# Optimization experiments

Measured on AMD Instinct MI355X. Metric: run time of the kernel, lower is better.

Reference implementation:

```python
import jax, jax.numpy as jnp
import numpy as np

B = 8192      # batch
F = 20        # sparse features
V = 1000      # vocab per sparse feature
E = 32        # embedding dim
ND = 10       # dense features
IN0 = (F + ND) * E  # 960 total embed dim
T = 2         # tasks
K = 4         # task experts per task
S = 4         # shared experts
D = 512       # expert dim
H = 256       # tower hidden
TEMP = 2.0    # gate temperature
EPS = 1e-5    # batchnorm eps


def setup_inputs() -> dict:
    key = jax.random.key(0)
    ks = iter(jax.random.split(key, 64))
    n = lambda shape, s=0.02: jax.random.normal(next(ks), shape, dtype=jnp.float32) * s
    inp = {
        'sparse_features': jax.random.randint(next(ks), (B, F), 0, V, dtype=jnp.int32),
        'dense_features': jax.random.normal(next(ks), (B, ND), dtype=jnp.float32),
        'emb_tables': n((F, V, E), 0.05),
        'dense_W': n((ND, ND * E)),
        'dense_b': jnp.zeros((ND * E,), jnp.float32),
    }
    for i, ind in enumerate([IN0, D, D]):
        inp[f'l{i}_Wt'] = n((T, K, ind, D))
        inp[f'l{i}_bt'] = jnp.zeros((T, K, D), jnp.float32)
        inp[f'l{i}_Ws'] = n((S, ind, D))
        inp[f'l{i}_bs'] = jnp.zeros((S, D), jnp.float32)
        inp[f'l{i}_Wg'] = n((T, ind, K + S))
        inp[f'l{i}_bg'] = jnp.zeros((T, K + S), jnp.float32)
    inp['tw1'] = n((T, D, H)); inp['tb1'] = jnp.zeros((T, H), jnp.float32)
    inp['bn_g'] = jnp.ones((T, H), jnp.float32); inp['bn_b'] = jnp.zeros((T, H), jnp.float32)
    inp['bn_m'] = jnp.zeros((T, H), jnp.float32); inp['bn_v'] = jnp.ones((T, H), jnp.float32)
    inp['tw2'] = n((T, H, H // 2)); inp['tb2'] = jnp.zeros((T, H // 2), jnp.float32)
    inp['tw3'] = n((T, H // 2)); inp['tb3'] = jnp.zeros((T,), jnp.float32)
    return inp


def _ple_layer(x, Wt, bt, Ws, bs, Wg, bg):
    # x: [B, in]; Wt: [T,K,in,D]; Ws: [S,in,D]; Wg: [T,in,K+S]
    shared = jax.nn.relu(jnp.einsum('bi,sio->bso', x, Ws) + bs)        # [B,S,D]
    task = jax.nn.relu(jnp.einsum('bi,tkio->btko', x, Wt) + bt)        # [B,T,K,D]
    Bn = x.shape[0]
    stack = jnp.concatenate(
        [task, jnp.broadcast_to(shared[:, None], (Bn, T) + shared.shape[1:])], axis=2)  # [B,T,K+S,D]
    gw = jax.nn.softmax((jnp.einsum('bi,tie->bte', x, Wg) + bg) / TEMP, axis=-1)        # [B,T,K+S]
    return jnp.einsum('bte,bted->btd', gw, stack)                      # [B,T,D]


def reference(sparse_features, dense_features, emb_tables, dense_W, dense_b,
              l0_Wt, l0_bt, l0_Ws, l0_bs, l0_Wg, l0_bg,
              l1_Wt, l1_bt, l1_Ws, l1_bs, l1_Wg, l1_bg,
              l2_Wt, l2_bt, l2_Ws, l2_bs, l2_Wg, l2_bg,
              tw1, tb1, bn_g, bn_b, bn_m, bn_v, tw2, tb2, tw3, tb3):
    # embedding: per-feature table lookup then concat with projected dense
    sp = emb_tables[jnp.arange(F)[None, :], sparse_features]           # [B,F,E]
    embed = jnp.concatenate(
        [sp.reshape(sp.shape[0], F * E), dense_features @ dense_W + dense_b], axis=1)  # [B,IN0]

    x = embed
    tout = None
    for (Wt, bt, Ws, bs, Wg, bg) in [
        (l0_Wt, l0_bt, l0_Ws, l0_bs, l0_Wg, l0_bg),
        (l1_Wt, l1_bt, l1_Ws, l1_bs, l1_Wg, l1_bg),
        (l2_Wt, l2_bt, l2_Ws, l2_bs, l2_Wg, l2_bg),
    ]:
        tout = _ple_layer(x, Wt, bt, Ws, bs, Wg, bg)   # [B,T,D]
        x = tout.mean(axis=1)                           # next layer input

    # task towers (eval mode: BN uses running stats, dropout off)
    h = jnp.einsum('btd,tdh->bth', tout, tw1) + tb1
    h = (h - bn_m) / jnp.sqrt(bn_v + EPS) * bn_g + bn_b
    h = jax.nn.relu(h)
    h = jax.nn.relu(jnp.einsum('bth,thg->btg', h, tw2) + tb2)
    logits = jnp.einsum('btg,tg->bt', h, tw3) + tb3     # [B,T]

    ctr = jax.nn.sigmoid(logits[:, 0])
    cvr_raw = jax.nn.sigmoid(logits[:, 1])
    ctcvr = ctr * cvr_raw
    # use_esmm=True -> cvr_pred == ctcvr
    return jnp.stack([ctr, ctcvr, ctcvr])               # [3,B]: ctr, cvr, ctcvr
```

## Files before the change

kernel.cpp:

```cpp
#include <hip/hip_runtime.h>
#include <math.h>

#define Bn 8192
#define INP0 960
#define Dn 512
#define Hn 256
#define TEMP_INV 0.5f

typedef __attribute__((ext_vector_type(8))) short short8;
typedef __attribute__((ext_vector_type(8))) unsigned short ushort8;
typedef __attribute__((ext_vector_type(4))) float f32x4;
typedef __attribute__((ext_vector_type(2))) long lx2;

__device__ __forceinline__ int swz(int x) { return x ^ ((x >> 3) & 0x70); }

__device__ __forceinline__ unsigned short f2bf(float f) {
  unsigned u = __builtin_bit_cast(unsigned, f);
  u += 0x7FFF + ((u >> 16) & 1);
  return (unsigned short)(u >> 16);
}
__device__ __forceinline__ float bf2f(unsigned short s) {
  unsigned u = ((unsigned)s) << 16;
  return __builtin_bit_cast(float, u);
}
__device__ __forceinline__ int pk4fp8(float a, float b, float c, float d) {
  int r = __builtin_amdgcn_cvt_pk_fp8_f32(a, b, 0, 0);
  r = __builtin_amdgcn_cvt_pk_fp8_f32(c, d, r, 1);
  return r;
}
__device__ __forceinline__ void gload16(const void* g, void* l) {
  __builtin_amdgcn_global_load_lds(
      (const __attribute__((address_space(1))) unsigned int*)g,
      (__attribute__((address_space(3))) unsigned int*)l, 16, 0, 0);
}

template <int IN>
__global__ __launch_bounds__(256) void conv_w(const float* __restrict__ Wt,
                                              const float* __restrict__ Ws,
                                              unsigned char* __restrict__ Wbt) {
  __shared__ float T[64][65];
  const int NK = IN / 64;
  int kk = blockIdx.x, dblk = blockIdx.y, e = blockIdx.z;
  int t = threadIdx.x;
  const float* base = (e < 8) ? (Wt + (size_t)e * IN * Dn) : (Ws + (size_t)(e - 8) * IN * Dn);
  int k = t >> 2, dg = t & 3;
  const float* gp = base + (size_t)(kk * 64 + k) * Dn + dblk * 64 + dg * 16;
#pragma unroll
  for (int i = 0; i < 4; ++i) {
    float4 v = *(const float4*)(gp + i * 4);
    T[dg * 16 + i * 4 + 0][k] = v.x;
    T[dg * 16 + i * 4 + 1][k] = v.y;
    T[dg * 16 + i * 4 + 2][k] = v.z;
    T[dg * 16 + i * 4 + 3][k] = v.w;
  }
  __syncthreads();
  int col = t >> 2, gq = t & 3;
  int g = gq ^ ((col >> 1) & 3);
  const float* Tc = T[col];
  int4 o;
  o.x = pk4fp8(Tc[g * 8 + 0] * 16.f, Tc[g * 8 + 1] * 16.f, Tc[g * 8 + 2] * 16.f, Tc[g * 8 + 3] * 16.f);
  o.y = pk4fp8(Tc[g * 8 + 4] * 16.f, Tc[g * 8 + 5] * 16.f, Tc[g * 8 + 6] * 16.f, Tc[g * 8 + 7] * 16.f);
  o.z = pk4fp8(Tc[32 + g * 8 + 0] * 16.f, Tc[32 + g * 8 + 1] * 16.f, Tc[32 + g * 8 + 2] * 16.f, Tc[32 + g * 8 + 3] * 16.f);
  o.w = pk4fp8(Tc[32 + g * 8 + 4] * 16.f, Tc[32 + g * 8 + 5] * 16.f, Tc[32 + g * 8 + 6] * 16.f, Tc[32 + g * 8 + 7] * 16.f);
  *(int4*)(Wbt + (((size_t)(dblk * NK + kk) * 12 + e) << 12) + t * 16) = o;
}

template <int K, int H>
__global__ __launch_bounds__(256) void conv_tw(const float* __restrict__ W,
                                               unsigned short* __restrict__ out) {
  __shared__ float T[64][33];
  int kk = blockIdx.x, hb = blockIdx.y, t = blockIdx.z;
  int tid = threadIdx.x;
  const float* base = W + (size_t)t * K * H;
  int k = tid >> 3, dq = tid & 7;
  const float* gp = base + (size_t)(kk * 32 + k) * H + hb * 64 + dq * 8;
  float4 v0 = *(const float4*)gp, v1 = *(const float4*)(gp + 4);
  T[dq * 8 + 0][k] = v0.x; T[dq * 8 + 1][k] = v0.y; T[dq * 8 + 2][k] = v0.z; T[dq * 8 + 3][k] = v0.w;
  T[dq * 8 + 4][k] = v1.x; T[dq * 8 + 5][k] = v1.y; T[dq * 8 + 6][k] = v1.z; T[dq * 8 + 7][k] = v1.w;
  __syncthreads();
  int L = tid * 16;
  int nat = swz(L);
  int c = nat >> 6, k0 = (nat & 63) >> 1;
  ushort8 o;
#pragma unroll
  for (int u = 0; u < 8; ++u) o[u] = f2bf(T[c][k0 + u]);
  const int NHB = H / 64;
  *(ushort8*)(out + (((size_t)(kk * NHB + hb) * 2 + t) << 11) + (L >> 1)) = o;
}

__global__ __launch_bounds__(256) void embed_kernel(
    const int* __restrict__ sparse, const float* __restrict__ dense,
    const float* __restrict__ emb, const float* __restrict__ dW,
    const float* __restrict__ db,
    unsigned short* __restrict__ xn, unsigned char* __restrict__ xt) {
  int b = blockIdx.x, t = threadIdx.x;
  __shared__ float dfs[10];
  if (t < 10) dfs[t] = dense[b * 10 + t];
  __syncthreads();
  if (t >= 240) return;
  int c = t * 4;
  float v[4];
  if (c < 640) {
    int f = c >> 5, e0 = c & 31;
    int idx = sparse[b * 20 + f];
    const float* ep = emb + ((size_t)f * 1000 + idx) * 32 + e0;
    float4 q = *(const float4*)ep;
    v[0] = q.x; v[1] = q.y; v[2] = q.z; v[3] = q.w;
  } else {
    int j = c - 640;
#pragma unroll
    for (int u = 0; u < 4; ++u) {
      float a = db[j + u];
#pragma unroll
      for (int d = 0; d < 10; ++d) a += dfs[d] * dW[d * 320 + j + u];
      v[u] = a;
    }
  }
  ushort4 pk;
  pk.x = f2bf(v[0]); pk.y = f2bf(v[1]); pk.z = f2bf(v[2]); pk.w = f2bf(v[3]);
  *(ushort4*)(xn + (size_t)b * 960 + c) = pk;
  int col = b & 63;
  int lc = c & 63;
  int ks = lc >> 5, g = (lc & 31) >> 3, j0 = lc & 7;
  int gq = g ^ ((col >> 1) & 3);
  int pos = (col << 6) + (gq << 4) + (ks << 3) + j0;
  int p8 = pk4fp8(v[0] * 16.f, v[1] * 16.f, v[2] * 16.f, v[3] * 16.f);
  *(int*)(xt + (((size_t)(c >> 6) * 128 + (b >> 6)) << 12) + pos) = p8;
}

template <int IN>
__global__ __launch_bounds__(256) void gate_kernel(
    const unsigned short* __restrict__ x, const float* __restrict__ Wg,
    const float* __restrict__ bg, float* __restrict__ gates) {
  int tid = threadIdx.x;
  int wv = tid >> 6, lane = tid & 63;
  int b = blockIdx.x * 4 + wv;
  int e = lane & 15, t = e >> 3, eg = e & 7;
  int slice = lane >> 4;
  const unsigned short* xr = x + (size_t)b * IN;
  const float* wr = Wg + (size_t)t * IN * 8 + eg;
  float p = 0.f;
  for (int i = slice * (IN / 4); i < (slice + 1) * (IN / 4); i += 4) {
    ushort4 xv = *(const ushort4*)(xr + i);
    p += bf2f(xv.x) * wr[(size_t)(i + 0) * 8];
    p += bf2f(xv.y) * wr[(size_t)(i + 1) * 8];
    p += bf2f(xv.z) * wr[(size_t)(i + 2) * 8];
    p += bf2f(xv.w) * wr[(size_t)(i + 3) * 8];
  }
  p += __shfl_xor(p, 32);
  p += __shfl_xor(p, 16);
  float z = (p + bg[t * 8 + eg]) * TEMP_INV;
  float m = z;
  m = fmaxf(m, __shfl_xor(m, 1)); m = fmaxf(m, __shfl_xor(m, 2)); m = fmaxf(m, __shfl_xor(m, 4));
  float ex = expf(z - m);
  float s = ex;
  s += __shfl_xor(s, 1); s += __shfl_xor(s, 2); s += __shfl_xor(s, 4);
  if (lane < 16) gates[(size_t)b * 16 + lane] = ex / s;
}

#define GSH 0
#define OUTS 4096
#define SB 22528
#define STG 53248

template <int IN, int MODE>
__global__ __launch_bounds__(768, 3) void ple_mfma(
    const unsigned char* __restrict__ xt, const float* __restrict__ gates,
    const unsigned char* __restrict__ Wbt,
    const float* __restrict__ btb, const float* __restrict__ bsh,
    unsigned short* __restrict__ outn, unsigned char* __restrict__ outt8,
    unsigned short* __restrict__ outtb) {
  __shared__ __align__(16) char smem[129024];
  const int NK = IN / 64;
  int tid = threadIdx.x;
  int wv = tid >> 6, lane = tid & 63;
  int r = lane & 15, g = lane >> 4;
  int s = blockIdx.x;
  int dblk = s & 7, bblk = s >> 3;
  int b0 = bblk * 64, d0 = dblk * 64;

  if (tid < 256)
    *(float4*)(smem + GSH + tid * 16) = *(const float4*)(gates + (size_t)b0 * 16 + tid * 4);

  f32x4 acc[4][4];
#pragma unroll
  for (int i = 0; i < 4; ++i)
#pragma unroll
    for (int j = 0; j < 4; ++j) acc[i][j] = f32x4{0.f, 0.f, 0.f, 0.f};

  const unsigned char* xchunk = xt + ((size_t)bblk << 12);
  const unsigned char* wchunk = Wbt + (size_t)(dblk * NK) * 49152;

  auto stage = [&](int t, char* lb) {
    const unsigned char* ws = wchunk + (size_t)t * 49152;
#pragma unroll
    for (int i = 0; i < 4; ++i)
      gload16(ws + tid * 16 + i * 12288, lb + tid * 16 + i * 12288);
    if (tid < 256)
      gload16(xchunk + (size_t)t * (128 * 4096) + tid * 16, lb + 49152 + tid * 16);
  };

  stage(0, smem + SB);

  for (int kk = 0; kk < NK; ++kk) {
    asm volatile("s_waitcnt vmcnt(0)" ::: "memory");
    __builtin_amdgcn_s_barrier();
    if (kk + 1 < NK) stage(kk + 1, smem + SB + ((kk + 1) & 1) * STG);
    {
      const char* lb = smem + SB + (kk & 1) * STG;
      const char* xb = lb + 49152;
      const char* wb = lb + (wv << 12);
      int base = (r << 6) + ((g ^ ((r >> 1) & 3)) << 4);
      lx2 A[4], B[4];
#pragma unroll
      for (int rt = 0; rt < 4; ++rt) A[rt] = *(const lx2*)(xb + rt * 1024 + base);
#pragma unroll
      for (int ct = 0; ct < 4; ++ct) B[ct] = *(const lx2*)(wb + ct * 1024 + base);
#pragma unroll
      for (int rt = 0; rt < 4; ++rt)
#pragma unroll
        for (int ct = 0; ct < 4; ++ct)
          acc[rt][ct] = __builtin_amdgcn_mfma_f32_16x16x32_fp8_fp8(A[rt][0], B[ct][0], acc[rt][ct], 0, 0, 0);
#pragma unroll
      for (int rt = 0; rt < 4; ++rt)
#pragma unroll
        for (int ct = 0; ct < 4; ++ct)
          acc[rt][ct] = __builtin_amdgcn_mfma_f32_16x16x32_fp8_fp8(A[rt][1], B[ct][1], acc[rt][ct], 0, 0, 0);
    }
  }
  __syncthreads();

  {
    const float* bp = (wv < 8) ? (btb + wv * Dn) : (bsh + (wv - 8) * Dn);
    float bias[4];
#pragma unroll
    for (int ct = 0; ct < 4; ++ct) bias[ct] = bp[d0 + ct * 16 + r];
    char* ex = smem + SB + (wv << 12);
#pragma unroll
    for (int rt = 0; rt < 4; ++rt)
#pragma unroll
      for (int ct = 0; ct < 4; ++ct) {
        float v0 = fmaxf(acc[rt][ct][0] * 0.00390625f + bias[ct], 0.f) * 16.f;
        float v1 = fmaxf(acc[rt][ct][1] * 0.00390625f + bias[ct], 0.f) * 16.f;
        float v2 = fmaxf(acc[rt][ct][2] * 0.00390625f + bias[ct], 0.f) * 16.f;
        float v3 = fmaxf(acc[rt][ct][3] * 0.00390625f + bias[ct], 0.f) * 16.f;
        int col = ct * 16 + r;
        int off = (col << 6) + rt * 16 + g * 4;
        off ^= (col & 7) << 3;
        *(int*)(ex + off) = pk4fp8(v0, v1, v2, v3);
      }
  }
  __syncthreads();

  if (tid < 512) {
    int col = tid & 63, q = tid >> 6;
    int exoff = ((col << 6) + (q << 3)) ^ ((col & 7) << 3);
    long v[12];
#pragma unroll
    for (int e = 0; e < 12; ++e)
      v[e] = *(const long*)(smem + SB + (e << 12) + exoff);
    unsigned short* os0 = (unsigned short*)(smem + OUTS);
    unsigned short* os1 = os0 + 64 * 72;
#pragma unroll
    for (int half = 0; half < 2; ++half) {
#pragma unroll
      for (int jj = 0; jj < 4; ++jj) {
        int row = (q << 3) + half * 4 + jj;
        const float* gp = (const float*)(smem + GSH + (row << 6));
        float4 ga = ((const float4*)gp)[0];
        float4 gb = ((const float4*)gp)[1];
        float4 gc = ((const float4*)gp)[2];
        float4 gd = ((const float4*)gp)[3];
        float f[12];
#pragma unroll
        for (int e = 0; e < 12; ++e) {
          unsigned w32 = (unsigned)(v[e] >> (half * 32));
          f[e] = __builtin_amdgcn_cvt_f32_fp8((int)(w32 >> (jj * 8)), 0);
        }
        float s0 = ga.x * f[0] + ga.y * f[1] + ga.z * f[2] + ga.w * f[3] +
                   gb.x * f[8] + gb.y * f[9] + gb.z * f[10] + gb.w * f[11];
        float s1 = gc.x * f[4] + gc.y * f[5] + gc.z * f[6] + gc.w * f[7] +
                   gd.x * f[8] + gd.y * f[9] + gd.z * f[10] + gd.w * f[11];
        os0[row * 72 + col] = f2bf(s0 * 0.0625f);
        os1[row * 72 + col] = f2bf(s1 * 0.0625f);
      }
    }
  }
  __syncthreads();

  if (tid < 512) {
    int row = tid >> 3, cq = tid & 7;
    const unsigned short* os0 = (const unsigned short*)(smem + OUTS) + row * 72 + cq * 8;
    const unsigned short* os1 = os0 + 64 * 72;
    ushort8 p0 = *(const ushort8*)os0, p1 = *(const ushort8*)os1;
    int b = b0 + row, d = d0 + cq * 8;
    if (MODE == 0) {
      float m[8];
      ushort8 pk;
#pragma unroll
      for (int u = 0; u < 8; ++u) {
        m[u] = 0.5f * (bf2f((unsigned short)p0[u]) + bf2f((unsigned short)p1[u]));
        pk[u] = f2bf(m[u]);
      }
      *(ushort8*)(outn + (size_t)b * Dn + d) = pk;
      int lk = d & 63;
      int ks = lk >> 5, g2 = (lk & 31) >> 3;
      int gq = g2 ^ ((row >> 1) & 3);
      int pos = (row << 6) + (gq << 4) + (ks << 3);
      int2 o8;
      o8.x = pk4fp8(m[0] * 16.f, m[1] * 16.f, m[2] * 16.f, m[3] * 16.f);
      o8.y = pk4fp8(m[4] * 16.f, m[5] * 16.f, m[6] * 16.f, m[7] * 16.f);
      *(int2*)(outt8 + (((size_t)dblk * 128 + bblk) << 12) + pos) = o8;
    } else {
      int kk2 = d >> 5;
      int nat = (row << 6) + ((d & 31) << 1);
      *(ushort8*)(outtb + (((size_t)(0 * 16 + kk2) * 128 + bblk) << 11) + (swz(nat) >> 1)) = p0;
      *(ushort8*)(outtb + (((size_t)(1 * 16 + kk2) * 128 + bblk) << 11) + (swz(nat) >> 1)) = p1;
    }
  }
}

#define TWBUF 36864
#define H1OFF 73728

__global__ __launch_bounds__(512) void tower_mfma(
    const unsigned short* __restrict__ toutT,
    const unsigned short* __restrict__ twbt1, const unsigned short* __restrict__ twbt2,
    const float* __restrict__ tb1,
    const float* __restrict__ bng, const float* __restrict__ bnb,
    const float* __restrict__ bnm, const float* __restrict__ bnv,
    const float* __restrict__ tb2, const float* __restrict__ tw3,
    const float* __restrict__ tb3, float* __restrict__ out) {
  __shared__ __align__(16) char smem[106496];
  int tid = threadIdx.x;
  int wv = tid >> 6, lane = tid & 63, r = lane & 15, g = lane >> 4;
  int blk = blockIdx.x;
  int bblk = blk >> 1, sub = blk & 1;
  int b0 = blk * 32;
  char* h1t = smem + H1OFF;

  int t1 = wv >> 2, hb = wv & 3;
  f32x4 acc[2][4];
#pragma unroll
  for (int i = 0; i < 2; ++i)
#pragma unroll
    for (int j = 0; j < 4; ++j) acc[i][j] = f32x4{0.f, 0.f, 0.f, 0.f};

  auto stage1 = [&](int t, char* lb) {
#pragma unroll
    for (int i = 0; i < 4; ++i)
      gload16((const char*)twbt1 + (size_t)t * 32768 + tid * 16 + i * 8192,
              lb + tid * 16 + i * 8192);
    if (tid < 256) {
      int tt = tid >> 7, off = (tid & 127) * 16;
      gload16((const char*)toutT + (((size_t)(tt * 16 + t) * 128 + bblk) << 12) + sub * 2048 + off,
              lb + 32768 + tt * 2048 + off);
    }
  };

  stage1(0, smem);
  __syncthreads();
  int cur = 0;
  for (int kk = 0; kk < 16; ++kk) {
    if (kk + 1 < 16) stage1(kk + 1, smem + (cur ^ 1) * TWBUF);
    {
      const char* lb = smem + cur * TWBUF;
      const char* wb = lb + (hb * 2 + t1) * 4096;
      const char* xb = lb + 32768 + t1 * 2048;
      short8 a[2], bfr[4];
#pragma unroll
      for (int rt = 0; rt < 2; ++rt)
        a[rt] = *(const short8*)(xb + swz(((rt * 16 + r) << 6) + (g << 4)));
#pragma unroll
      for (int ct = 0; ct < 4; ++ct)
        bfr[ct] = *(const short8*)(wb + swz(((ct * 16 + r) << 6) + (g << 4)));
#pragma unroll
      for (int rt = 0; rt < 2; ++rt)
#pragma unroll
        for (int ct = 0; ct < 4; ++ct)
          acc[rt][ct] = __builtin_amdgcn_mfma_f32_16x16x32_bf16(a[rt], bfr[ct], acc[rt][ct], 0, 0, 0);
    }
    __syncthreads();
    cur ^= 1;
  }

  {
#pragma unroll
    for (int ct = 0; ct < 4; ++ct) {
      int h = hb * 64 + ct * 16 + r;
      int idx = t1 * 256 + h;
      float inv = rsqrtf(bnv[idx] + 1e-5f) * bng[idx];
      float mu = bnm[idx], be = bnb[idx], bias = tb1[idx];
      int kk2 = h >> 5, kloc = h & 31;
      char* tile = h1t + (t1 * 8 + kk2) * 2048;
#pragma unroll
      for (int rt = 0; rt < 2; ++rt)
#pragma unroll
        for (int j = 0; j < 4; ++j) {
          int lr = rt * 16 + g * 4 + j;
          float v = acc[rt][ct][j] + bias;
          v = (v - mu) * inv + be;
          v = fmaxf(v, 0.f);
          *(unsigned short*)(tile + swz((lr << 6) + (kloc << 1))) = f2bf(v);
        }
    }
  }
  __syncthreads();

  float* h2x = (float*)smem;
  if (wv < 4) {
    int t2 = wv >> 1, hb2 = wv & 1;
    f32x4 acc2[2][4];
#pragma unroll
    for (int i = 0; i < 2; ++i)
#pragma unroll
      for (int j = 0; j < 4; ++j) acc2[i][j] = f32x4{0.f, 0.f, 0.f, 0.f};
    for (int kk = 0; kk < 8; ++kk) {
      const char* xb = h1t + (t2 * 8 + kk) * 2048;
      const char* wb = (const char*)twbt2 + ((kk * 2 + hb2) * 2 + t2) * 4096;
      short8 a[2], bfr[4];
#pragma unroll
      for (int rt = 0; rt < 2; ++rt)
        a[rt] = *(const short8*)(xb + swz(((rt * 16 + r) << 6) + (g << 4)));
#pragma unroll
      for (int ct = 0; ct < 4; ++ct)
        bfr[ct] = *(const short8*)(wb + swz(((ct * 16 + r) << 6) + (g << 4)));
#pragma unroll
      for (int rt = 0; rt < 2; ++rt)
#pragma unroll
        for (int ct = 0; ct < 4; ++ct)
          acc2[rt][ct] = __builtin_amdgcn_mfma_f32_16x16x32_bf16(a[rt], bfr[ct], acc2[rt][ct], 0, 0, 0);
    }
#pragma unroll
    for (int ct = 0; ct < 4; ++ct) {
      int col = hb2 * 64 + ct * 16 + r;
      float bias = tb2[t2 * 128 + col];
#pragma unroll
      for (int rt = 0; rt < 2; ++rt)
#pragma unroll
        for (int j = 0; j < 4; ++j) {
          int lr = rt * 16 + g * 4 + j;
          h2x[(t2 * 32 + lr) * 129 + col] = fmaxf(acc2[rt][ct][j] + bias, 0.f);
        }
    }
  }
  __syncthreads();

  float* lgs = (float*)(smem + 40960);
  if (tid < 64) {
    int t3 = tid >> 5, lr = tid & 31;
    const float* hr = h2x + (t3 * 32 + lr) * 129;
    const float* w3 = tw3 + t3 * 128;
    float s = 0.f;
#pragma unroll 8
    for (int i = 0; i < 128; ++i) s += hr[i] * w3[i];
    lgs[t3 * 32 + lr] = s + tb3[t3];
  }
  __syncthreads();
  if (tid < 32) {
    int b = b0 + tid;
    float ctr = 1.f / (1.f + expf(-lgs[tid]));
    float cvr = 1.f / (1.f + expf(-lgs[32 + tid]));
    float cc = ctr * cvr;
    out[b] = ctr;
    out[Bn + b] = cc;
    out[2 * Bn + b] = cc;
  }
}

extern "C" void kernel_launch(void* const* d_in, const int* in_sizes, int n_in,
                              void* d_out, int out_size, void* d_ws, size_t ws_size,
                              hipStream_t stream) {
  const int* sparse   = (const int*)d_in[0];
  const float* dense  = (const float*)d_in[1];
  const float* emb    = (const float*)d_in[2];
  const float* dW     = (const float*)d_in[3];
  const float* db     = (const float*)d_in[4];
  const float* Wt[3]  = {(const float*)d_in[5],  (const float*)d_in[11], (const float*)d_in[17]};
  const float* btb[3] = {(const float*)d_in[6],  (const float*)d_in[12], (const float*)d_in[18]};
  const float* Wsh[3] = {(const float*)d_in[7],  (const float*)d_in[13], (const float*)d_in[19]};
  const float* bsh[3] = {(const float*)d_in[8],  (const float*)d_in[14], (const float*)d_in[20]};
  const float* Wg[3]  = {(const float*)d_in[9],  (const float*)d_in[15], (const float*)d_in[21]};
  const float* bg[3]  = {(const float*)d_in[10], (const float*)d_in[16], (const float*)d_in[22]};
  const float* tw1 = (const float*)d_in[23];
  const float* tb1 = (const float*)d_in[24];
  const float* bng = (const float*)d_in[25];
  const float* bnb = (const float*)d_in[26];
  const float* bnm = (const float*)d_in[27];
  const float* bnv = (const float*)d_in[28];
  const float* tw2 = (const float*)d_in[29];
  const float* tb2 = (const float*)d_in[30];
  const float* tw3 = (const float*)d_in[31];
  const float* tb3 = (const float*)d_in[32];

  unsigned short* x0n = (unsigned short*)d_ws;
  unsigned short* x1n = x0n + (size_t)Bn * 960;
  unsigned short* toutT = x1n + (size_t)Bn * 512;
  float* gatesB = (float*)(toutT + (size_t)Bn * 1024);
  unsigned short* twbt1 = (unsigned short*)(gatesB + (size_t)Bn * 16);
  unsigned short* twbt2 = twbt1 + (size_t)2 * 512 * 256;
  unsigned char* x0t = (unsigned char*)(twbt2 + (size_t)2 * 256 * 128);
  unsigned char* x1t = x0t + (size_t)Bn * 960;
  unsigned char* Wbt = x1t + (size_t)Bn * 512;
  unsigned short* x2n = x0n;
  unsigned char* x2t = x0t;

  conv_tw<512, 256><<<dim3(16, 4, 2), 256, 0, stream>>>(tw1, twbt1);
  conv_tw<256, 128><<<dim3(8, 2, 2), 256, 0, stream>>>(tw2, twbt2);

  conv_w<960><<<dim3(15, 8, 12), 256, 0, stream>>>(Wt[0], Wsh[0], Wbt);
  embed_kernel<<<Bn, 256, 0, stream>>>(sparse, dense, emb, dW, db, x0n, x0t);
  gate_kernel<960><<<Bn / 4, 256, 0, stream>>>(x0n, Wg[0], bg[0], gatesB);
  ple_mfma<960, 0><<<1024, 768, 0, stream>>>(x0t, gatesB, Wbt, btb[0], bsh[0], x1n, x1t, nullptr);

  conv_w<512><<<dim3(8, 8, 12), 256, 0, stream>>>(Wt[1], Wsh[1], Wbt);
  gate_kernel<512><<<Bn / 4, 256, 0, stream>>>(x1n, Wg[1], bg[1], gatesB);
  ple_mfma<512, 0><<<1024, 768, 0, stream>>>(x1t, gatesB, Wbt, btb[1], bsh[1], x2n, x2t, nullptr);

  conv_w<512><<<dim3(8, 8, 12), 256, 0, stream>>>(Wt[2], Wsh[2], Wbt);
  gate_kernel<512><<<Bn / 4, 256, 0, stream>>>(x2n, Wg[2], bg[2], gatesB);
  ple_mfma<512, 1><<<1024, 768, 0, stream>>>(x2t, gatesB, Wbt, btb[2], bsh[2], nullptr, nullptr, toutT);

  tower_mfma<<<256, 512, 0, stream>>>(toutT, twbt1, twbt2, tb1, bng, bnb, bnm, bnv,
                                      tb2, tw3, tb3, (float*)d_out);
}
```

Measured before the change: 296.7 us.

## Pre-transpose gate weights to bf16, batch embed rows, use bf16 expert staging

```diff
diff --git a/kernel.cpp b/kernel.cpp
--- a/kernel.cpp
+++ b/kernel.cpp
@@ -63,6 +63,14 @@
   o.z = pk4fp8(Tc[32 + g * 8 + 0] * 16.f, Tc[32 + g * 8 + 1] * 16.f, Tc[32 + g * 8 + 2] * 16.f, Tc[32 + g * 8 + 3] * 16.f);
   o.w = pk4fp8(Tc[32 + g * 8 + 4] * 16.f, Tc[32 + g * 8 + 5] * 16.f, Tc[32 + g * 8 + 6] * 16.f, Tc[32 + g * 8 + 7] * 16.f);
   *(int4*)(Wbt + (((size_t)(dblk * NK + kk) * 12 + e) << 12) + t * 16) = o;
+}
+
+__global__ __launch_bounds__(64) void conv_wg(const float* __restrict__ Wg,
+                                              unsigned short* __restrict__ out, int IN) {
+  int i = blockIdx.x * 64 + threadIdx.x;
+  int e = blockIdx.y;
+  int t = e >> 3, eg = e & 7;
+  if (i < IN) out[(size_t)e * IN + i] = f2bf(Wg[((size_t)t * IN + i) * 8 + eg]);
 }
 
 template <int K, int H>
@@ -93,62 +101,67 @@
     const float* __restrict__ emb, const float* __restrict__ dW,
     const float* __restrict__ db,
     unsigned short* __restrict__ xn, unsigned char* __restrict__ xt) {
-  int b = blockIdx.x, t = threadIdx.x;
-  __shared__ float dfs[10];
-  if (t < 10) dfs[t] = dense[b * 10 + t];
+  int b0 = blockIdx.x * 4, t = threadIdx.x;
+  __shared__ float dfs[4][10];
+  if (t < 40) dfs[t / 10][t % 10] = dense[(b0 + t / 10) * 10 + t % 10];
   __syncthreads();
   if (t >= 240) return;
   int c = t * 4;
-  float v[4];
-  if (c < 640) {
-    int f = c >> 5, e0 = c & 31;
-    int idx = sparse[b * 20 + f];
-    const float* ep = emb + ((size_t)f * 1000 + idx) * 32 + e0;
-    float4 q = *(const float4*)ep;
-    v[0] = q.x; v[1] = q.y; v[2] = q.z; v[3] = q.w;
-  } else {
-    int j = c - 640;
-#pragma unroll
-    for (int u = 0; u < 4; ++u) {
-      float a = db[j + u];
-#pragma unroll
-      for (int d = 0; d < 10; ++d) a += dfs[d] * dW[d * 320 + j + u];
-      v[u] = a;
-    }
-  }
-  ushort4 pk;
-  pk.x = f2bf(v[0]); pk.y = f2bf(v[1]); pk.z = f2bf(v[2]); pk.w = f2bf(v[3]);
-  *(ushort4*)(xn + (size_t)b * 960 + c) = pk;
-  int col = b & 63;
-  int lc = c & 63;
-  int ks = lc >> 5, g = (lc & 31) >> 3, j0 = lc & 7;
-  int gq = g ^ ((col >> 1) & 3);
-  int pos = (col << 6) + (gq << 4) + (ks << 3) + j0;
-  int p8 = pk4fp8(v[0] * 16.f, v[1] * 16.f, v[2] * 16.f, v[3] * 16.f);
-  *(int*)(xt + (((size_t)(c >> 6) * 128 + (b >> 6)) << 12) + pos) = p8;
+#pragma unroll 1
+  for (int r = 0; r < 4; ++r) {
+    int b = b0 + r;
+    float v[4];
+    if (c < 640) {
+      int f = c >> 5, e0 = c & 31;
+      int idx = sparse[b * 20 + f];
+      const float* ep = emb + ((size_t)f * 1000 + idx) * 32 + e0;
+      float4 q = *(const float4*)ep;
+      v[0] = q.x; v[1] = q.y; v[2] = q.z; v[3] = q.w;
+    } else {
+      int j = c - 640;
+#pragma unroll
+      for (int u = 0; u < 4; ++u) {
+        float a = db[j + u];
+#pragma unroll
+        for (int d = 0; d < 10; ++d) a += dfs[r][d] * dW[d * 320 + j + u];
+        v[u] = a;
+      }
+    }
+    ushort4 pk;
+    pk.x = f2bf(v[0]); pk.y = f2bf(v[1]); pk.z = f2bf(v[2]); pk.w = f2bf(v[3]);
+    *(ushort4*)(xn + (size_t)b * 960 + c) = pk;
+    int col = b & 63;
+    int lc = c & 63;
+    int ks = lc >> 5, g = (lc & 31) >> 3, j0 = lc & 7;
+    int gq = g ^ ((col >> 1) & 3);
+    int pos = (col << 6) + (gq << 4) + (ks << 3) + j0;
+    int p8 = pk4fp8(v[0] * 16.f, v[1] * 16.f, v[2] * 16.f, v[3] * 16.f);
+    *(int*)(xt + (((size_t)(c >> 6) * 128 + (b >> 6)) << 12) + pos) = p8;
+  }
 }
 
 template <int IN>
 __global__ __launch_bounds__(256) void gate_kernel(
-    const unsigned short* __restrict__ x, const float* __restrict__ Wg,
+    const unsigned short* __restrict__ x, const unsigned short* __restrict__ wgb,
     const float* __restrict__ bg, float* __restrict__ gates) {
   int tid = threadIdx.x;
   int wv = tid >> 6, lane = tid & 63;
   int b = blockIdx.x * 4 + wv;
-  int e = lane & 15, t = e >> 3, eg = e & 7;
-  int slice = lane >> 4;
-  const unsigned short* xr = x + (size_t)b * IN;
-  const float* wr = Wg + (size_t)t * IN * 8 + eg;
+  int e = lane & 15, slice = lane >> 4;
+  const unsigned short* xr = x + (size_t)b * IN + slice * (IN / 4);
+  const unsigned short* wr = wgb + (size_t)e * IN + slice * (IN / 4);
   float p = 0.f;
-  for (int i = slice * (IN / 4); i < (slice + 1) * (IN / 4); i += 4) {
-    ushort4 xv = *(const ushort4*)(xr + i);
-    p += bf2f(xv.x) * wr[(size_t)(i + 0) * 8];
-    p += bf2f(xv.y) * wr[(size_t)(i + 1) * 8];
-    p += bf2f(xv.z) * wr[(size_t)(i + 2) * 8];
-    p += bf2f(xv.w) * wr[(size_t)(i + 3) * 8];
-  }
+#pragma unroll 2
+  for (int i = 0; i < IN / 4; i += 8) {
+    short8 xv = *(const short8*)(xr + i);
+    short8 wv2 = *(const short8*)(wr + i);
+#pragma unroll
+    for (int u = 0; u < 8; ++u)
+      p += bf2f((unsigned short)xv[u]) * bf2f((unsigned short)wv2[u]);
+  }
+  p += __shfl_xor(p, 16);
   p += __shfl_xor(p, 32);
-  p += __shfl_xor(p, 16);
+  int t = e >> 3, eg = e & 7;
   float z = (p + bg[t * 8 + eg]) * TEMP_INV;
   float m = z;
   m = fmaxf(m, __shfl_xor(m, 1)); m = fmaxf(m, __shfl_xor(m, 2)); m = fmaxf(m, __shfl_xor(m, 4));
@@ -235,55 +248,50 @@
     float bias[4];
 #pragma unroll
     for (int ct = 0; ct < 4; ++ct) bias[ct] = bp[d0 + ct * 16 + r];
-    char* ex = smem + SB + (wv << 12);
+    char* ex = smem + SB + (wv << 13);
 #pragma unroll
     for (int rt = 0; rt < 4; ++rt)
 #pragma unroll
       for (int ct = 0; ct < 4; ++ct) {
-        float v0 = fmaxf(acc[rt][ct][0] * 0.00390625f + bias[ct], 0.f) * 16.f;
-        float v1 = fmaxf(acc[rt][ct][1] * 0.00390625f + bias[ct], 0.f) * 16.f;
-        float v2 = fmaxf(acc[rt][ct][2] * 0.00390625f + bias[ct], 0.f) * 16.f;
-        float v3 = fmaxf(acc[rt][ct][3] * 0.00390625f + bias[ct], 0.f) * 16.f;
+        float v0 = fmaxf(acc[rt][ct][0] * 0.00390625f + bias[ct], 0.f);
+        float v1 = fmaxf(acc[rt][ct][1] * 0.00390625f + bias[ct], 0.f);
+        float v2 = fmaxf(acc[rt][ct][2] * 0.00390625f + bias[ct], 0.f);
+        float v3 = fmaxf(acc[rt][ct][3] * 0.00390625f + bias[ct], 0.f);
+        uint2 pk;
+        pk.x = (unsigned)f2bf(v0) | ((unsigned)f2bf(v1) << 16);
+        pk.y = (unsigned)f2bf(v2) | ((unsigned)f2bf(v3) << 16);
         int col = ct * 16 + r;
-        int off = (col << 6) + rt * 16 + g * 4;
-        off ^= (col & 7) << 3;
-        *(int*)(ex + off) = pk4fp8(v0, v1, v2, v3);
+        *(uint2*)(ex + swz(col * 128 + rt * 32 + g * 8)) = pk;
       }
   }
   __syncthreads();
 
   if (tid < 512) {
     int col = tid & 63, q = tid >> 6;
-    int exoff = ((col << 6) + (q << 3)) ^ ((col & 7) << 3);
-    long v[12];
+    short8 v[12];
 #pragma unroll
     for (int e = 0; e < 12; ++e)
-      v[e] = *(const long*)(smem + SB + (e << 12) + exoff);
+      v[e] = *(const short8*)(smem + SB + (e << 13) + swz(col * 128 + q * 16));
     unsigned short* os0 = (unsigned short*)(smem + OUTS);
     unsigned short* os1 = os0 + 64 * 72;
 #pragma unroll
-    for (int half = 0; half < 2; ++half) {
-#pragma unroll
-      for (int jj = 0; jj < 4; ++jj) {
-        int row = (q << 3) + half * 4 + jj;
-        const float* gp = (const float*)(smem + GSH + (row << 6));
-        float4 ga = ((const float4*)gp)[0];
-        float4 gb = ((const float4*)gp)[1];
-        float4 gc = ((const float4*)gp)[2];
-        float4 gd = ((const float4*)gp)[3];
-        float f[12];
-#pragma unroll
-        for (int e = 0; e < 12; ++e) {
-          unsigned w32 = (unsigned)(v[e] >> (half * 32));
-          f[e] = __builtin_amdgcn_cvt_f32_fp8((int)(w32 >> (jj * 8)), 0);
-        }
-        float s0 = ga.x * f[0] + ga.y * f[1] + ga.z * f[2] + ga.w * f[3] +
-                   gb.x * f[8] + gb.y * f[9] + gb.z * f[10] + gb.w * f[11];
-        float s1 = gc.x * f[4] + gc.y * f[5] + gc.z * f[6] + gc.w * f[7] +
-                   gd.x * f[8] + gd.y * f[9] + gd.z * f[10] + gd.w * f[11];
-        os0[row * 72 + col] = f2bf(s0 * 0.0625f);
-        os1[row * 72 + col] = f2bf(s1 * 0.0625f);
-      }
+    for (int jj = 0; jj < 8; ++jj) {
+      int row = q * 8 + jj;
+      const float* gp = (const float*)(smem + GSH + (row << 6));
+      float4 ga = ((const float4*)gp)[0];
+      float4 gb = ((const float4*)gp)[1];
+      float4 gc = ((const float4*)gp)[2];
+      float4 gd = ((const float4*)gp)[3];
+      float sh0 = bf2f((unsigned short)v[8][jj]), sh1 = bf2f((unsigned short)v[9][jj]);
+      float sh2 = bf2f((unsigned short)v[10][jj]), sh3 = bf2f((unsigned short)v[11][jj]);
+      float s0 = ga.x * bf2f((unsigned short)v[0][jj]) + ga.y * bf2f((unsigned short)v[1][jj]) +
+                 ga.z * bf2f((unsigned short)v[2][jj]) + ga.w * bf2f((unsigned short)v[3][jj]) +
+                 gb.x * sh0 + gb.y * sh1 + gb.z * sh2 + gb.w * sh3;
+      float s1 = gc.x * bf2f((unsigned short)v[4][jj]) + gc.y * bf2f((unsigned short)v[5][jj]) +
+                 gc.z * bf2f((unsigned short)v[6][jj]) + gc.w * bf2f((unsigned short)v[7][jj]) +
+                 gd.x * sh0 + gd.y * sh1 + gd.z * sh2 + gd.w * sh3;
+      os0[row * 72 + col] = f2bf(s0);
+      os1[row * 72 + col] = f2bf(s1);
     }
   }
   __syncthreads();
@@ -502,23 +510,29 @@
   unsigned char* x0t = (unsigned char*)(twbt2 + (size_t)2 * 256 * 128);
   unsigned char* x1t = x0t + (size_t)Bn * 960;
   unsigned char* Wbt = x1t + (size_t)Bn * 512;
+  unsigned short* wgb0 = (unsigned short*)(Wbt + (size_t)6 * 1024 * 1024);
+  unsigned short* wgb1 = wgb0 + (size_t)16 * 960;
+  unsigned short* wgb2 = wgb1 + (size_t)16 * 512;
   unsigned short* x2n = x0n;
   unsigned char* x2t = x0t;
 
   conv_tw<512, 256><<<dim3(16, 4, 2), 256, 0, stream>>>(tw1, twbt1);
   conv_tw<256, 128><<<dim3(8, 2, 2), 256, 0, stream>>>(tw2, twbt2);
+  conv_wg<<<dim3(15, 16), 64, 0, stream>>>(Wg[0], wgb0, 960);
+  conv_wg<<<dim3(8, 16), 64, 0, stream>>>(Wg[1], wgb1, 512);
+  conv_wg<<<dim3(8, 16), 64, 0, stream>>>(Wg[2], wgb2, 512);
 
   conv_w<960><<<dim3(15, 8, 12), 256, 0, stream>>>(Wt[0], Wsh[0], Wbt);
-  embed_kernel<<<Bn, 256, 0, stream>>>(sparse, dense, emb, dW, db, x0n, x0t);
-  gate_kernel<960><<<Bn / 4, 256, 0, stream>>>(x0n, Wg[0], bg[0], gatesB);
+  embed_kernel<<<Bn / 4, 256, 0, stream>>>(sparse, dense, emb, dW, db, x0n, x0t);
+  gate_kernel<960><<<Bn / 4, 256, 0, stream>>>(x0n, wgb0, bg[0], gatesB);
   ple_mfma<960, 0><<<1024, 768, 0, stream>>>(x0t, gatesB, Wbt, btb[0], bsh[0], x1n, x1t, nullptr);
 
   conv_w<512><<<dim3(8, 8, 12), 256, 0, stream>>>(Wt[1], Wsh[1], Wbt);
-  gate_kernel<512><<<Bn / 4, 256, 0, stream>>>(x1n, Wg[1], bg[1], gatesB);
+  gate_kernel<512><<<Bn / 4, 256, 0, stream>>>(x1n, wgb1, bg[1], gatesB);
   ple_mfma<512, 0><<<1024, 768, 0, stream>>>(x1t, gatesB, Wbt, btb[1], bsh[1], x2n, x2t, nullptr);
 
   conv_w<512><<<dim3(8, 8, 12), 256, 0, stream>>>(Wt[2], Wsh[2], Wbt);
-  gate_kernel<512><<<Bn / 4, 256, 0, stream>>>(x2n, Wg[2], bg[2], gatesB);
+  gate_kernel<512><<<Bn / 4, 256, 0, stream>>>(x2n, wgb2, bg[2], gatesB);
   ple_mfma<512, 1><<<1024, 768, 0, stream>>>(x2t, gatesB, Wbt, btb[2], bsh[2], nullptr, nullptr, toutT);
 
   tower_mfma<<<256, 512, 0, stream>>>(toutT, twbt1, twbt2, tb1, bng, bnb, bnm, bnv,
```

Result: no change. 302.0 us (+1.8%).
